# Optimization experiments

Measured on AMD Instinct MI355X. Metric: run time of the kernel, lower is better.

Reference implementation:

```python
import jax, jax.numpy as jnp
import numpy as np

D_MODEL = 1024
HEADS = 4
DK = 1024          # key_dim = d_model * expand_k
DV = 2048          # value_dim = d_model * expand_v
HDK = DK // HEADS  # 256
HDV = DV // HEADS  # 512
LOW_RANK = 16
CHUNK = 64
GATE_NORM = 16.0
EPS = 1e-5


def setup_inputs() -> dict:
    key = jax.random.key(0)
    ks = jax.random.split(key, 10)
    gain = 2.0 ** (-2.5)

    def xavier(k, shape):  # shape = (fan_in, fan_out); stored as [in, out]
        lim = gain * np.sqrt(6.0 / (shape[0] + shape[1]))
        return jax.random.uniform(k, shape, jnp.float32, -lim, lim)

    return {
        'x': jax.random.normal(ks[0], (2, 2048, D_MODEL), jnp.float32),
        'Wq': xavier(ks[1], (D_MODEL, DK)),
        'Wk': xavier(ks[2], (D_MODEL, DK)),
        'Wv': xavier(ks[3], (D_MODEL, DV)),
        'Wg': xavier(ks[4], (D_MODEL, DV)),
        'Wgk1': xavier(ks[5], (D_MODEL, LOW_RANK)),
        'Wgk2': xavier(ks[6], (LOW_RANK, DK)),
        'bgk2': jnp.zeros((DK,), jnp.float32),
        'Wo': xavier(ks[7], (DV, D_MODEL)),
        'rms_w': jnp.ones((HDV,), jnp.float32),
    }


def _gla_chunked(q, k, v, g):
    """Gated linear attention: S_t = exp(g_t) (*) S_{t-1} + k_t^T v_t;  o_t = scale * q_t @ S_t.
    q,k,g: [B,H,T,HDK]; v: [B,H,T,HDV]. Chunk-parallel formulation, scan over chunks."""
    B, H, T, _ = q.shape
    NC = T // CHUNK
    scale = HDK ** -0.5

    def to_chunks(t, d):  # [B,H,T,d] -> [NC,B,H,CHUNK,d]
        return t.reshape(B, H, NC, CHUNK, d).transpose(2, 0, 1, 3, 4)

    qc = to_chunks(q, HDK)
    kc = to_chunks(k, HDK)
    vc = to_chunks(v, HDV)
    bc = jnp.cumsum(to_chunks(g, HDK), axis=-2)  # inclusive log-decay within chunk
    mask = jnp.tril(jnp.ones((CHUNK, CHUNK), bool))

    def step(S, inp):
        qb, kb, vb, bb = inp                       # [B,H,C,HDK/HDV]
        qg = qb * jnp.exp(bb) * scale              # queries decayed to chunk start
        kd = kb * jnp.exp(-bb)                     # keys un-decayed (intra)
        A = jnp.einsum('bhtd,bhsd->bhts', qg, kd)  # intra-chunk scores
        A = jnp.where(mask, A, 0.0)
        o = jnp.einsum('bhts,bhsv->bhtv', A, vb) + jnp.einsum('bhtd,bhdv->bhtv', qg, S)
        b_last = bb[:, :, -1:, :]                  # [B,H,1,HDK]
        kg = kb * jnp.exp(b_last - bb)             # keys decayed to chunk end
        S = S * jnp.exp(b_last[:, :, 0, :])[..., None] + jnp.einsum('bhtd,bhtv->bhdv', kg, vb)
        return S, o

    S0 = jnp.zeros((B, H, HDK, HDV), q.dtype)
    _, o = jax.lax.scan(step, S0, (qc, kc, vc, bc))  # o: [NC,B,H,C,HDV]
    return o.transpose(1, 2, 0, 3, 4).reshape(B, H, T, HDV)


def reference(x, Wq, Wk, Wv, Wg, Wgk1, Wgk2, bgk2, Wo, rms_w):
    B, T, _ = x.shape
    q = (x @ Wq).reshape(B, T, HEADS, HDK).transpose(0, 2, 1, 3)
    k = (x @ Wk).reshape(B, T, HEADS, HDK).transpose(0, 2, 1, 3)
    v = (x @ Wv).reshape(B, T, HEADS, HDV).transpose(0, 2, 1, 3)
    gk = (x @ Wgk1) @ Wgk2 + bgk2                       # low-rank gate logits
    g = jax.nn.log_sigmoid(gk.astype(jnp.float32)) / GATE_NORM
    g = g.reshape(B, T, HEADS, HDK).transpose(0, 2, 1, 3)

    o = _gla_chunked(q, k, v, g)                        # [B,H,T,HDV]
    o = o.transpose(0, 2, 1, 3)                         # [B,T,H,HDV]
    o = o * jax.lax.rsqrt(jnp.mean(o * o, axis=-1, keepdims=True) + EPS) * rms_w
    o = o.reshape(B, T, HEADS * HDV)
    o = o * jax.nn.silu(x @ Wg)
    return o @ Wo
```

## Files before the change

### kernel.cpp

```cpp
#include <hip/hip_runtime.h>
#include <hip/hip_bf16.h>
#include <math.h>

#define TOK  4096
#define DM   1024
#define DKC  1024
#define DVC  2048
#define NH   4
#define HDK_ 256
#define HDV_ 512
#define NCH  32
#define CHK  64

typedef __attribute__((ext_vector_type(8))) short bf16x8;
typedef __attribute__((ext_vector_type(4))) float f32x4;

__device__ inline float bf2f(short s) {
    unsigned int b = ((unsigned int)(unsigned short)s) << 16;
    return __uint_as_float(b);
}
__device__ inline short f2bf_bits(float f) {
    __hip_bfloat16 h = __float2bfloat16(f);
    return *reinterpret_cast<short*>(&h);
}

__device__ __forceinline__ void gl_lds16(const void* g, void* l) {
    __builtin_amdgcn_global_load_lds((const __attribute__((address_space(1))) void*)g,
                                     (__attribute__((address_space(3))) void*)l, 16, 0, 0);
}

__global__ __launch_bounds__(256) void prep_all(const float* __restrict__ Wq,
                                                const float* __restrict__ Wk,
                                                const float* __restrict__ Wv,
                                                const float* __restrict__ Wg,
                                                const float* __restrict__ Wo,
                                                __hip_bfloat16* __restrict__ WtAll,
                                                __hip_bfloat16* __restrict__ WtO,
                                                const float* __restrict__ x,
                                                const float* __restrict__ W1,
                                                const float* __restrict__ W2,
                                                const float* __restrict__ b2,
                                                __hip_bfloat16* __restrict__ xb,
                                                float* __restrict__ g) {
    const int bid = blockIdx.x;
    const int tid = threadIdx.x;
    if (bid < 8192) {
        __shared__ float tile[32][33];
        const float* W; __hip_bfloat16* Wt; int K, N, r;
        if (bid < 1024)      { W = Wq; Wt = WtAll;               K = 1024; N = 1024; r = bid; }
        else if (bid < 2048) { W = Wk; Wt = WtAll + 1024 * 1024; K = 1024; N = 1024; r = bid - 1024; }
        else if (bid < 4096) { W = Wv; Wt = WtAll + 2048 * 1024; K = 1024; N = 2048; r = bid - 2048; }
        else if (bid < 6144) { W = Wg; Wt = WtAll + 4096 * 1024; K = 1024; N = 2048; r = bid - 4096; }
        else                 { W = Wo; Wt = WtO;                 K = 2048; N = 1024; r = bid - 6144; }
        const int ncols = N >> 5;
        const int n0 = (r % ncols) * 32, k0 = (r / ncols) * 32;
        const int tx = tid & 31, ty = tid >> 5;
#pragma unroll
        for (int i = 0; i < 32; i += 8)
            tile[ty + i][tx] = W[(size_t)(k0 + ty + i) * N + n0 + tx];
        __syncthreads();
#pragma unroll
        for (int i = 0; i < 32; i += 8)
            Wt[(size_t)(n0 + ty + i) * K + k0 + tx] = __float2bfloat16(tile[tx][ty + i]);
    } else {
        __shared__ float xl[1024];
        __shared__ float red[16][17];
        __shared__ float t1l[16];
        const int t = bid - 8192;
        float4 xv = *reinterpret_cast<const float4*>(&x[(size_t)t * DM + tid * 4]);
        *reinterpret_cast<float4*>(&xl[tid * 4]) = xv;
        short4 xs;
        xs.x = f2bf_bits(xv.x); xs.y = f2bf_bits(xv.y);
        xs.z = f2bf_bits(xv.z); xs.w = f2bf_bits(xv.w);
        *reinterpret_cast<short4*>((short*)xb + (size_t)t * DM + tid * 4) = xs;
        __syncthreads();
        const int o = tid & 15, p = tid >> 4;
        float s = 0.f;
#pragma unroll 8
        for (int m = 0; m < 64; ++m) {
            int kk = p * 64 + m;
            s += xl[kk] * W1[kk * 16 + o];
        }
        red[p][o] = s;
        __syncthreads();
        if (tid < 16) {
            float tot = 0.f;
#pragma unroll
            for (int pp = 0; pp < 16; ++pp) tot += red[pp][tid];
            t1l[tid] = tot;
        }
        __syncthreads();
#pragma unroll
        for (int j = 0; j < 4; ++j) {
            int c = tid + j * 256;
            float acc = b2[c];
#pragma unroll
            for (int r2 = 0; r2 < 16; ++r2) acc += t1l[r2] * W2[r2 * 1024 + c];
            float ls = fminf(acc, 0.f) - log1pf(expf(-fabsf(acc)));
            g[(size_t)t * DKC + c] = ls * (1.f / 16.f);
        }
    }
}

__global__ __launch_bounds__(512) void gemm256(const __hip_bfloat16* __restrict__ A,
                                               const __hip_bfloat16* __restrict__ Wt,
                                               __hip_bfloat16* __restrict__ qo,
                                               __hip_bfloat16* __restrict__ ko,
                                               __hip_bfloat16* __restrict__ vT,
                                               __hip_bfloat16* __restrict__ xgo) {
    __shared__ __align__(16) short SM[9 * 8192];
    const int K = 1024, NT = 16;
    const int tid = threadIdx.x;
    const int wave = tid >> 6, lane = tid & 63;
    const int wr = wave >> 2;
    const int wc = wave & 3;
    const int hc = wc >> 1;
    const int l15 = lane & 15, kb = lane >> 4;
    const int m0 = blockIdx.y * 128, n0 = blockIdx.x * 256;

    const bool isV = (n0 >= 2048 && n0 < 4096);
    __hip_bfloat16* dst = nullptr; int ldd = 0, nloc0 = 0;
    if (n0 < 1024)       { dst = qo;  ldd = 1024; nloc0 = n0; }
    else if (n0 < 2048)  { dst = ko;  ldd = 1024; nloc0 = n0 - 1024; }
    else if (n0 >= 4096) { dst = xgo; ldd = 2048; nloc0 = n0 - 4096; }

    f32x4 acc[4][4];
#pragma unroll
    for (int mf = 0; mf < 4; ++mf)
#pragma unroll
        for (int nf = 0; nf < 4; ++nf) acc[mf][nf] = (f32x4){0.f, 0.f, 0.f, 0.f};

    auto stage_unit = [&](int u) {
        int tk = u / 3, p = u % 3;
        int slot = u % 9;
#pragma unroll
        for (int j = 0; j < 2; ++j) {
            int row = (wave * 2 + j) * 8 + (lane >> 3);
            int srcg = (lane & 7) ^ (row & 7);
            const __hip_bfloat16* src =
                (p == 0) ? &A[(size_t)(m0 + row) * K + tk * 64 + srcg * 8]
                         : &Wt[(size_t)(n0 + (p - 1) * 128 + row) * K + tk * 64 + srcg * 8];
            gl_lds16(src, &SM[slot * 8192 + (wave * 2 + j) * 512]);
        }
    };

    for (int u = 0; u <= 5; ++u) stage_unit(u);

    const int ULAST = 3 * NT - 1;
    for (int t = 0; t < NT; ++t) {
        if (t < NT - 1) asm volatile("s_waitcnt vmcnt(6)" ::: "memory");
        else            asm volatile("s_waitcnt vmcnt(0)" ::: "memory");
        __builtin_amdgcn_sched_barrier(0);
        __builtin_amdgcn_s_barrier();

        if (3 * t + 6 <= ULAST) stage_unit(3 * t + 6);
        if (3 * t + 7 <= ULAST) stage_unit(3 * t + 7);
        if (3 * t + 8 <= ULAST) stage_unit(3 * t + 8);
        __builtin_amdgcn_sched_barrier(0);

        const short* Abase = &SM[((3 * t) % 9) * 8192];
        const short* Bbase = &SM[((3 * t + 1 + hc) % 9) * 8192];

        bf16x8 a0[4], b0[4], a1[4], b1[4];
#pragma unroll
        for (int mf = 0; mf < 4; ++mf) {
            int row = wr * 64 + mf * 16 + l15;
            a0[mf] = *reinterpret_cast<const bf16x8*>(&Abase[row * 64 + (kb ^ (row & 7)) * 8]);
        }
#pragma unroll
        for (int nf = 0; nf < 4; ++nf) {
            int row = (wc & 1) * 64 + nf * 16 + l15;
            b0[nf] = *reinterpret_cast<const bf16x8*>(&Bbase[row * 64 + (kb ^ (row & 7)) * 8]);
        }
        __builtin_amdgcn_sched_barrier(0);
#pragma unroll
        for (int mf = 0; mf < 4; ++mf) {
            int row = wr * 64 + mf * 16 + l15;
            a1[mf] = *reinterpret_cast<const bf16x8*>(&Abase[row * 64 + ((4 + kb) ^ (row & 7)) * 8]);
        }
#pragma unroll
        for (int nf = 0; nf < 4; ++nf) {
            int row = (wc & 1) * 64 + nf * 16 + l15;
            b1[nf] = *reinterpret_cast<const bf16x8*>(&Bbase[row * 64 + ((4 + kb) ^ (row & 7)) * 8]);
        }
        __builtin_amdgcn_sched_barrier(0);
        asm volatile("s_waitcnt lgkmcnt(8)" ::: "memory");
        __builtin_amdgcn_sched_barrier(0);
        __builtin_amdgcn_s_setprio(1);
#pragma unroll
        for (int mf = 0; mf < 4; ++mf)
#pragma unroll
            for (int nf = 0; nf < 4; ++nf)
                acc[mf][nf] = __builtin_amdgcn_mfma_f32_16x16x32_bf16(a0[mf], b0[nf], acc[mf][nf], 0, 0, 0);
        __builtin_amdgcn_s_setprio(0);
        asm volatile("s_waitcnt lgkmcnt(0)" ::: "memory");
        __builtin_amdgcn_sched_barrier(0);
        __builtin_amdgcn_s_setprio(1);
#pragma unroll
        for (int mf = 0; mf < 4; ++mf)
#pragma unroll
            for (int nf = 0; nf < 4; ++nf)
                acc[mf][nf] = __builtin_amdgcn_mfma_f32_16x16x32_bf16(a1[mf], b1[nf], acc[mf][nf], 0, 0, 0);
        __builtin_amdgcn_s_setprio(0);
    }

    if (!isV) {
#pragma unroll
        for (int mf = 0; mf < 4; ++mf)
#pragma unroll
            for (int nf = 0; nf < 4; ++nf)
#pragma unroll
                for (int r = 0; r < 4; ++r)
                    dst[(size_t)(m0 + wr * 64 + mf * 16 + kb * 4 + r) * ldd +
                        nloc0 + wc * 64 + nf * 16 + l15] = __float2bfloat16(acc[mf][nf][r]);
    } else {
        __syncthreads();
        short* Cl = SM;
#pragma unroll
        for (int mf = 0; mf < 4; ++mf)
#pragma unroll
            for (int nf = 0; nf < 4; ++nf)
#pragma unroll
                for (int r = 0; r < 4; ++r) {
                    int trow = wr * 64 + mf * 16 + kb * 4 + r;
                    int vcol = wc * 64 + nf * 16 + l15;
                    Cl[vcol * 132 + trow] = f2bf_bits(acc[mf][nf][r]);
                }
        __syncthreads();
        const int vcg0 = n0 - 2048;
        const int bh = (m0 >> 11) * NH + (vcg0 >> 9);
        const int vl0 = vcg0 & 511;
        const int tl0 = m0 & 2047;
        short* vTs = (short*)vT;
#pragma unroll
        for (int it = 0; it < 8; ++it) {
            int idx = tid + it * 512;
            int row = idx >> 4;
            int c8 = (idx & 15) * 8;
            bf16x8 vv = *reinterpret_cast<const bf16x8*>(&Cl[row * 132 + c8]);
            *reinterpret_cast<bf16x8*>(
                &vTs[((size_t)(bh * 512 + vl0 + row)) * 2048 + tl0 + c8]) = vv;
        }
    }
}

__global__ __launch_bounds__(256) void gemm_bf16(const __hip_bfloat16* __restrict__ A,
                                                 const __hip_bfloat16* __restrict__ Wt,
                                                 float* __restrict__ C,
                                                 int M, int N, int K) {
    __shared__ __align__(16) short Buf[2][2][128 * 64];
    const int tid = threadIdx.x;
    const int wave = tid >> 6, lane = tid & 63;
    const int wr = wave >> 1, wc = wave & 1;
    const int m0 = blockIdx.y * 128, n0 = blockIdx.x * 128;
    const int l15 = lane & 15, kb = lane >> 4;
    const int lr8 = lane >> 3, lc8 = (lane & 7) * 8;
    const int NT = K >> 6;

    f32x4 acc[4][4];
#pragma unroll
    for (int mf = 0; mf < 4; ++mf)
#pragma unroll
        for (int nf = 0; nf < 4; ++nf) acc[mf][nf] = (f32x4){0.f, 0.f, 0.f, 0.f};

#define STAGE_G(kt, bi)                                                          \
    {                                                                            \
        int k0s = (kt) * 64;                                                     \
        _Pragma("unroll")                                                        \
        for (int j = 0; j < 4; ++j) {                                            \
            int inst = wave * 4 + j;                                             \
            int r = inst * 8 + lr8;                                              \
            gl_lds16(&A[(size_t)(m0 + r) * K + k0s + lc8], &Buf[bi][0][inst * 512]); \
            gl_lds16(&Wt[(size_t)(n0 + r) * K + k0s + lc8], &Buf[bi][1][inst * 512]); \
        }                                                                        \
    }

    STAGE_G(0, 0);
    STAGE_G(1, 1);

    for (int t = 0; t < NT; ++t) {
        if (t + 1 < NT) asm volatile("s_waitcnt vmcnt(8)" ::: "memory");
        else            asm volatile("s_waitcnt vmcnt(0)" ::: "memory");
        __builtin_amdgcn_sched_barrier(0);
        __builtin_amdgcn_s_barrier();
        const short* Ab = Buf[t & 1][0];
        const short* Bb = Buf[t & 1][1];
        bf16x8 a0[4], b0[4], a1[4], b1[4];
#pragma unroll
        for (int mf = 0; mf < 4; ++mf)
            a0[mf] = *reinterpret_cast<const bf16x8*>(&Ab[(wr * 64 + mf * 16 + l15) * 64 + kb * 8]);
#pragma unroll
        for (int nf = 0; nf < 4; ++nf)
            b0[nf] = *reinterpret_cast<const bf16x8*>(&Bb[(wc * 64 + nf * 16 + l15) * 64 + kb * 8]);
        __builtin_amdgcn_sched_barrier(0);
#pragma unroll
        for (int mf = 0; mf < 4; ++mf)
            a1[mf] = *reinterpret_cast<const bf16x8*>(&Ab[(wr * 64 + mf * 16 + l15) * 64 + 32 + kb * 8]);
#pragma unroll
        for (int nf = 0; nf < 4; ++nf)
            b1[nf] = *reinterpret_cast<const bf16x8*>(&Bb[(wc * 64 + nf * 16 + l15) * 64 + 32 + kb * 8]);
        __builtin_amdgcn_sched_barrier(0);
        asm volatile("s_waitcnt lgkmcnt(8)" ::: "memory");
        __builtin_amdgcn_sched_barrier(0);
#pragma unroll
        for (int mf = 0; mf < 4; ++mf)
#pragma unroll
            for (int nf = 0; nf < 4; ++nf)
                acc[mf][nf] = __builtin_amdgcn_mfma_f32_16x16x32_bf16(a0[mf], b0[nf], acc[mf][nf], 0, 0, 0);
        asm volatile("s_waitcnt lgkmcnt(0)" ::: "memory");
        __builtin_amdgcn_sched_barrier(0);
#pragma unroll
        for (int mf = 0; mf < 4; ++mf)
#pragma unroll
            for (int nf = 0; nf < 4; ++nf)
                acc[mf][nf] = __builtin_amdgcn_mfma_f32_16x16x32_bf16(a1[mf], b1[nf], acc[mf][nf], 0, 0, 0);
        __builtin_amdgcn_sched_barrier(0);
        __builtin_amdgcn_s_barrier();
        if (t + 2 < NT) STAGE_G(t + 2, t & 1);
    }
#undef STAGE_G

#pragma unroll
    for (int mf = 0; mf < 4; ++mf)
#pragma unroll
        for (int nf = 0; nf < 4; ++nf)
#pragma unroll
            for (int r = 0; r < 4; ++r)
                C[(size_t)(m0 + wr * 64 + mf * 16 + kb * 4 + r) * N + n0 + wc * 64 + nf * 16 + l15] =
                    acc[mf][nf][r];
}

__global__ __launch_bounds__(256) void gla_chunk(const __hip_bfloat16* __restrict__ qb,
                                                 const __hip_bfloat16* __restrict__ kb,
                                                 const __hip_bfloat16* __restrict__ vT,
                                                 const float* __restrict__ g,
                                                 __hip_bfloat16* __restrict__ qg,
                                                 __hip_bfloat16* __restrict__ U,
                                                 __hip_bfloat16* __restrict__ o1,
                                                 float* __restrict__ dlast) {
    __shared__ __align__(16) short SM[53248];
    short* qg_l = SM;
    short* kd_l = SM + 16384;
    short* V_l  = SM;
    short* kg_l = SM + 32768;
    short* Am_l = SM + 49152;

    const int chunk = blockIdx.x, bh = blockIdx.y;
    const int b = bh >> 2, h = bh & 3;
    const int t0 = b * 2048 + chunk * 64;
    const int tt0 = chunk * 64;
    const int tid = threadIdx.x;
    const float scale = 0.0625f;

    {
        const int d = tid;
        const float* gcol = g + (size_t)t0 * DKC + h * HDK_ + d;
        const __hip_bfloat16* qcol = qb + (size_t)t0 * DKC + h * HDK_ + d;
        const __hip_bfloat16* kcol = kb + (size_t)t0 * DKC + h * HDK_ + d;
        float run = 0.f;
#pragma unroll
        for (int i = 0; i < 64; ++i) run += gcol[(size_t)i * DKC];
        const float ebl = expf(run);
        dlast[((size_t)bh * NCH + chunk) * HDK_ + d] = ebl;

        bf16x8 kreg[8];
        run = 0.f;
#pragma unroll
        for (int i = 0; i < 64; ++i) {
            run += gcol[(size_t)i * DKC];
            float eb = expf(run);
            float qv = __bfloat162float(qcol[(size_t)i * DKC]) * eb * scale;
            float kdv = __bfloat162float(kcol[(size_t)i * DKC]) * expf(-run);
            qg[(size_t)(t0 + i) * DKC + h * HDK_ + d] = __float2bfloat16(qv);
            int bq = ((i * 512 + d * 2) ^ ((i & 7) << 4)) >> 1;
            qg_l[bq] = f2bf_bits(qv);
            kd_l[bq] = f2bf_bits(kdv);
            kreg[i >> 3][i & 7] = f2bf_bits(kdv * ebl);
        }
#pragma unroll
        for (int j = 0; j < 8; ++j)
            *reinterpret_cast<bf16x8*>(&kg_l[d * 64 + ((j ^ (d & 7)) * 8)]) = kreg[j];
    }
    __syncthreads();

    const int wv = tid >> 6, lane = tid & 63;
    const int l15 = lane & 15, kb_ = lane >> 4;

    {
        f32x4 accA[4];
#pragma unroll
        for (int sf = 0; sf < 4; ++sf) accA[sf] = (f32x4){0.f, 0.f, 0.f, 0.f};
        const int trow = wv * 16 + l15;
#pragma unroll
        for (int ks = 0; ks < 8; ++ks) {
            bf16x8 af = *reinterpret_cast<const bf16x8*>(
                &qg_l[((trow * 512 + (ks * 32 + kb_ * 8) * 2) ^ ((trow & 7) << 4)) >> 1]);
#pragma unroll
            for (int sf = 0; sf < 4; ++sf) {
                int srow = sf * 16 + l15;
                bf16x8 bfr = *reinterpret_cast<const bf16x8*>(
                    &kd_l[((srow * 512 + (ks * 32 + kb_ * 8) * 2) ^ ((srow & 7) << 4)) >> 1]);
                accA[sf] = __builtin_amdgcn_mfma_f32_16x16x32_bf16(af, bfr, accA[sf], 0, 0, 0);
            }
        }
#pragma unroll
        for (int sf = 0; sf < 4; ++sf)
#pragma unroll
            for (int r = 0; r < 4; ++r) {
                int t = wv * 16 + kb_ * 4 + r, s = sf * 16 + l15;
                float val = (t >= s) ? accA[sf][r] : 0.f;
                Am_l[((t * 128 + s * 2) ^ ((t & 7) << 4)) >> 1] = f2bf_bits(val);
            }
    }
    __syncthreads();

    {
        const int lr8 = lane >> 3, slot = lane & 7;
#pragma unroll
        for (int i8 = 0; i8 < 16; ++i8) {
            int vrow0 = wv * 128 + i8 * 8;
            const __hip_bfloat16* src =
                &vT[((size_t)bh * 512 + vrow0 + lr8) * 2048 + tt0 + (slot ^ (lr8 & 7)) * 8];
            gl_lds16(src, &V_l[vrow0 * 64]);
        }
    }
    __syncthreads();

    {
        f32x4 accO[4][8];
#pragma unroll
        for (int tf = 0; tf < 4; ++tf)
#pragma unroll
            for (int vf = 0; vf < 8; ++vf) accO[tf][vf] = (f32x4){0.f, 0.f, 0.f, 0.f};
#pragma unroll
        for (int kk = 0; kk < 2; ++kk) {
            bf16x8 af[4];
#pragma unroll
            for (int tf = 0; tf < 4; ++tf) {
                int row = tf * 16 + l15;
                af[tf] = *reinterpret_cast<const bf16x8*>(
                    &Am_l[((row * 128 + (kk * 32 + kb_ * 8) * 2) ^ ((row & 7) << 4)) >> 1]);
            }
#pragma unroll
            for (int vf = 0; vf < 8; ++vf) {
                int rv = wv * 128 + vf * 16 + l15;
                bf16x8 bfr = *reinterpret_cast<const bf16x8*>(
                    &V_l[((rv * 128 + (kk * 32 + kb_ * 8) * 2) ^ ((rv & 7) << 4)) >> 1]);
#pragma unroll
                for (int tf = 0; tf < 4; ++tf)
                    accO[tf][vf] = __builtin_amdgcn_mfma_f32_16x16x32_bf16(af[tf], bfr, accO[tf][vf], 0, 0, 0);
            }
        }
#pragma unroll
        for (int tf = 0; tf < 4; ++tf)
#pragma unroll
            for (int vf = 0; vf < 8; ++vf)
#pragma unroll
                for (int r = 0; r < 4; ++r) {
                    int t = tf * 16 + kb_ * 4 + r;
                    int vv = wv * 128 + vf * 16 + l15;
                    o1[(size_t)(t0 + t) * DVC + h * HDV_ + vv] = __float2bfloat16(accO[tf][vf][r]);
                }
    }

    {
        const size_t Ub = ((size_t)bh * NCH + chunk) * 131072;
        for (int d0 = 0; d0 < 256; d0 += 64) {
            f32x4 accU[8][4];
#pragma unroll
            for (int vf = 0; vf < 8; ++vf)
#pragma unroll
                for (int nf = 0; nf < 4; ++nf) accU[vf][nf] = (f32x4){0.f, 0.f, 0.f, 0.f};
#pragma unroll
            for (int kk = 0; kk < 2; ++kk) {
                bf16x8 av[8], bv[4];
#pragma unroll
                for (int vf = 0; vf < 8; ++vf) {
                    int rv = wv * 128 + vf * 16 + l15;
                    av[vf] = *reinterpret_cast<const bf16x8*>(
                        &V_l[((rv * 128 + (kk * 32 + kb_ * 8) * 2) ^ ((rv & 7) << 4)) >> 1]);
                }
#pragma unroll
                for (int nf = 0; nf < 4; ++nf) {
                    int row = d0 + nf * 16 + l15;
                    bv[nf] = *reinterpret_cast<const bf16x8*>(
                        &kg_l[row * 64 + (((kk * 4 + kb_) ^ (row & 7)) * 8)]);
                }
#pragma unroll
                for (int vf = 0; vf < 8; ++vf)
#pragma unroll
                    for (int nf = 0; nf < 4; ++nf)
                        accU[vf][nf] = __builtin_amdgcn_mfma_f32_16x16x32_bf16(av[vf], bv[nf], accU[vf][nf], 0, 0, 0);
            }
#pragma unroll
            for (int vf = 0; vf < 8; ++vf)
#pragma unroll
                for (int nf = 0; nf < 4; ++nf)
#pragma unroll
                    for (int r = 0; r < 4; ++r) {
                        int vc = wv * 128 + vf * 16 + kb_ * 4 + r;
                        int d = d0 + nf * 16 + l15;
                        U[Ub + (size_t)vc * 256 + d] = __float2bfloat16(accU[vf][nf][r]);
                    }
        }
    }
}

__global__ __launch_bounds__(256) void scan_pass(__hip_bfloat16* __restrict__ U,
                                                 const float* __restrict__ dlast) {
    int gid = blockIdx.x * 256 + threadIdx.x;
    int bh = gid >> 14;
    int rem = gid & 16383;
    int vc = rem >> 5;
    int dg = rem & 31;
    float S[8];
#pragma unroll
    for (int j = 0; j < 8; ++j) S[j] = 0.f;
    size_t base = (size_t)bh * NCH * 131072 + (size_t)vc * 256 + dg * 8;
    for (int c = 0; c < NCH; ++c) {
        __hip_bfloat16* p = U + base + (size_t)c * 131072;
        bf16x8 u = *reinterpret_cast<bf16x8*>(p);
        const float* dl = &dlast[((size_t)bh * NCH + c) * HDK_ + dg * 8];
        float4 e0 = *reinterpret_cast<const float4*>(dl);
        float4 e1 = *reinterpret_cast<const float4*>(dl + 4);
        float e[8] = {e0.x, e0.y, e0.z, e0.w, e1.x, e1.y, e1.z, e1.w};
        bf16x8 outv;
#pragma unroll
        for (int j = 0; j < 8; ++j) {
            outv[j] = f2bf_bits(S[j]);
            S[j] = S[j] * e[j] + bf2f(u[j]);
        }
        *reinterpret_cast<bf16x8*>(p) = outv;
    }
}

__global__ __launch_bounds__(256) void o_pass(const __hip_bfloat16* __restrict__ qg,
                                              const __hip_bfloat16* __restrict__ U,
                                              const __hip_bfloat16* __restrict__ o1,
                                              __hip_bfloat16* __restrict__ o2) {
    __shared__ __align__(16) char smem[64 * 132 * 4];
    short* Av = (short*)smem;
    short* Bv = (short*)smem + 128 * 64;
    float* oT = (float*)smem;
    const int vt = blockIdx.x, c = blockIdx.y, bh = blockIdx.z;
    const int b = bh >> 2, h = bh & 3;
    const int vc0 = vt * 128;
    const int t0 = b * 2048 + c * 64;
    const int tid = threadIdx.x;
    const int wave = tid >> 6, lane = tid & 63;
    const int wr = wave >> 1, wc = wave & 1;
    const int l15 = lane & 15, kb = lane >> 4;
    const int lr8 = lane >> 3, lc8 = (lane & 7) * 8;
    const size_t Ub = ((size_t)bh * NCH + c) * 131072;

    f32x4 acc[4][2];
#pragma unroll
    for (int mf = 0; mf < 4; ++mf)
#pragma unroll
        for (int nf = 0; nf < 2; ++nf) acc[mf][nf] = (f32x4){0.f, 0.f, 0.f, 0.f};

    for (int ks = 0; ks < 4; ++ks) {
        const int d0 = ks * 64;
#pragma unroll
        for (int j = 0; j < 4; ++j) {
            int inst = wave * 4 + j;
            int r = inst * 8 + lr8;
            gl_lds16(&U[Ub + (size_t)(vc0 + r) * 256 + d0 + lc8], &Av[inst * 512]);
        }
#pragma unroll
        for (int j = 0; j < 2; ++j) {
            int inst = wave * 2 + j;
            int r = inst * 8 + lr8;
            gl_lds16(&qg[(size_t)(t0 + r) * DKC + h * HDK_ + d0 + lc8], &Bv[inst * 512]);
        }
        __syncthreads();
#pragma unroll
        for (int kk = 0; kk < 2; ++kk) {
            bf16x8 af[4], bfr[2];
#pragma unroll
            for (int mf = 0; mf < 4; ++mf)
                af[mf] = *reinterpret_cast<const bf16x8*>(&Av[(wr * 64 + mf * 16 + l15) * 64 + kk * 32 + kb * 8]);
#pragma unroll
            for (int nf = 0; nf < 2; ++nf)
                bfr[nf] = *reinterpret_cast<const bf16x8*>(&Bv[(wc * 32 + nf * 16 + l15) * 64 + kk * 32 + kb * 8]);
#pragma unroll
            for (int mf = 0; mf < 4; ++mf)
#pragma unroll
                for (int nf = 0; nf < 2; ++nf)
                    acc[mf][nf] = __builtin_amdgcn_mfma_f32_16x16x32_bf16(af[mf], bfr[nf], acc[mf][nf], 0, 0, 0);
        }
        __syncthreads();
    }
#pragma unroll
    for (int mf = 0; mf < 4; ++mf)
#pragma unroll
        for (int nf = 0; nf < 2; ++nf)
#pragma unroll
            for (int r = 0; r < 4; ++r)
                oT[(wc * 32 + nf * 16 + l15) * 132 + wr * 64 + mf * 16 + kb * 4 + r] = acc[mf][nf][r];
    __syncthreads();
#pragma unroll
    for (int j = 0; j < 4; ++j) {
        int t = (tid >> 4) + j * 16;
        int vc8 = (tid & 15) * 8;
        float4 a0 = *reinterpret_cast<const float4*>(&oT[t * 132 + vc8]);
        float4 a1 = *reinterpret_cast<const float4*>(&oT[t * 132 + vc8 + 4]);
        size_t oi = (size_t)(t0 + t) * DVC + h * HDV_ + vc0 + vc8;
        bf16x8 iv = *reinterpret_cast<const bf16x8*>(&o1[oi]);
        bf16x8 outv;
        outv[0] = f2bf_bits(a0.x + bf2f(iv[0]));
        outv[1] = f2bf_bits(a0.y + bf2f(iv[1]));
        outv[2] = f2bf_bits(a0.z + bf2f(iv[2]));
        outv[3] = f2bf_bits(a0.w + bf2f(iv[3]));
        outv[4] = f2bf_bits(a1.x + bf2f(iv[4]));
        outv[5] = f2bf_bits(a1.y + bf2f(iv[5]));
        outv[6] = f2bf_bits(a1.z + bf2f(iv[6]));
        outv[7] = f2bf_bits(a1.w + bf2f(iv[7]));
        *reinterpret_cast<bf16x8*>((__hip_bfloat16*)o2 + oi) = outv;
    }
}

__global__ __launch_bounds__(256) void rms_gate(const __hip_bfloat16* __restrict__ o2,
                                                const __hip_bfloat16* __restrict__ xg,
                                                const float* __restrict__ rms_w,
                                                __hip_bfloat16* __restrict__ gated) {
    __shared__ float wsum[4];
    const int th = blockIdx.x;
    const int t = th >> 2, h = th & 3;
    const int tid = threadIdx.x;
    const size_t base = (size_t)t * DVC + h * HDV_;
    short2 ov = reinterpret_cast<const short2*>((const short*)o2 + base)[tid];
    float v0 = bf2f(ov.x), v1 = bf2f(ov.y);
    float s = v0 * v0 + v1 * v1;
#pragma unroll
    for (int off = 32; off >= 1; off >>= 1) s += __shfl_down(s, off, 64);
    if ((tid & 63) == 0) wsum[tid >> 6] = s;
    __syncthreads();
    float tot = wsum[0] + wsum[1] + wsum[2] + wsum[3];
    float rms = rsqrtf(tot * (1.f / 512.f) + 1e-5f);
    short2 gv = reinterpret_cast<const short2*>((const short*)xg + base)[tid];
    float g0 = bf2f(gv.x), g1 = bf2f(gv.y);
    float s0 = g0 / (1.f + expf(-g0));
    float s1 = g1 / (1.f + expf(-g1));
    float2 w = reinterpret_cast<const float2*>(rms_w)[tid];
    short2 outp;
    outp.x = f2bf_bits(v0 * rms * w.x * s0);
    outp.y = f2bf_bits(v1 * rms * w.y * s1);
    reinterpret_cast<short2*>((short*)gated + base)[tid] = outp;
}

extern "C" void kernel_launch(void* const* d_in, const int* in_sizes, int n_in,
                              void* d_out, int out_size, void* d_ws, size_t ws_size,
                              hipStream_t stream) {
    const float* x    = (const float*)d_in[0];
    const float* Wq   = (const float*)d_in[1];
    const float* Wk   = (const float*)d_in[2];
    const float* Wv   = (const float*)d_in[3];
    const float* Wg   = (const float*)d_in[4];
    const float* Wgk1 = (const float*)d_in[5];
    const float* Wgk2 = (const float*)d_in[6];
    const float* bgk2 = (const float*)d_in[7];
    const float* Wo   = (const float*)d_in[8];
    const float* rmsw = (const float*)d_in[9];
    float* out = (float*)d_out;
    float* ws = (float*)d_ws;

    const size_t M1 = 1ull << 20;
    __hip_bfloat16* xb    = (__hip_bfloat16*)ws;
    __hip_bfloat16* WtAll = (__hip_bfloat16*)(ws + 2 * M1);
    __hip_bfloat16* q_b   = (__hip_bfloat16*)(ws + 5 * M1);
    __hip_bfloat16* k_b   = (__hip_bfloat16*)(ws + 7 * M1);
    float*          g     = ws + 13 * M1;
    __hip_bfloat16* U     = (__hip_bfloat16*)ws;
    __hip_bfloat16* xg_b  = (__hip_bfloat16*)(ws + 17 * M1);
    __hip_bfloat16* qgb   = (__hip_bfloat16*)(ws + 21 * M1);
    __hip_bfloat16* vT    = (__hip_bfloat16*)(ws + 25 * M1);
    __hip_bfloat16* o1    = (__hip_bfloat16*)(ws + 29 * M1);
    __hip_bfloat16* o2    = (__hip_bfloat16*)(ws + 33 * M1);
    float*          dlast = ws + 37 * M1 + 65536;
    __hip_bfloat16* WtO   = (__hip_bfloat16*)(ws + 38 * M1);
    __hip_bfloat16* gated = (__hip_bfloat16*)(ws + 25 * M1);

    prep_all<<<12288, 256, 0, stream>>>(Wq, Wk, Wv, Wg, Wo, WtAll, WtO,
                                        x, Wgk1, Wgk2, bgk2, xb, g);

    gemm256<<<dim3(24, 32), 512, 0, stream>>>(xb, WtAll, q_b, k_b, vT, xg_b);

    gla_chunk<<<dim3(NCH, 8), 256, 0, stream>>>(q_b, k_b, vT, g, qgb, U, o1, dlast);

    scan_pass<<<512, 256, 0, stream>>>(U, dlast);
    o_pass<<<dim3(4, NCH, 8), 256, 0, stream>>>(qgb, U, o1, o2);

    rms_gate<<<TOK * NH, 256, 0, stream>>>(o2, xg_b, rmsw, gated);
    gemm_bf16<<<dim3(8, 32), 256, 0, stream>>>(gated, WtO, out, TOK, DM, DVC);
}
```

Before: 224.5 us.

## Fuse inter-chunk output pass with RMS norm and SiLU gating

```diff
diff --git a/kernel.cpp b/kernel.cpp
--- a/kernel.cpp
+++ b/kernel.cpp
@@ -534,17 +534,18 @@
     }
 }
 
-__global__ __launch_bounds__(256) void o_pass(const __hip_bfloat16* __restrict__ qg,
+__global__ __launch_bounds__(256) void o_gate(const __hip_bfloat16* __restrict__ qg,
                                               const __hip_bfloat16* __restrict__ U,
                                               const __hip_bfloat16* __restrict__ o1,
-                                              __hip_bfloat16* __restrict__ o2) {
-    __shared__ __align__(16) char smem[64 * 132 * 4];
-    short* Av = (short*)smem;
-    short* Bv = (short*)smem + 128 * 64;
-    float* oT = (float*)smem;
-    const int vt = blockIdx.x, c = blockIdx.y, bh = blockIdx.z;
+                                              const __hip_bfloat16* __restrict__ xg,
+                                              const float* __restrict__ rms_w,
+                                              __hip_bfloat16* __restrict__ gated) {
+    __shared__ __align__(16) short Av[128 * 64];
+    __shared__ __align__(16) short Bv[64 * 64];
+    __shared__ __align__(16) short oT[64 * 520];
+    __shared__ float red[64][4];
+    const int c = blockIdx.x, bh = blockIdx.y;
     const int b = bh >> 2, h = bh & 3;
-    const int vc0 = vt * 128;
     const int t0 = b * 2048 + c * 64;
     const int tid = threadIdx.x;
     const int wave = tid >> 6, lane = tid & 63;
@@ -553,100 +554,102 @@
     const int lr8 = lane >> 3, lc8 = (lane & 7) * 8;
     const size_t Ub = ((size_t)bh * NCH + c) * 131072;
 
-    f32x4 acc[4][2];
-#pragma unroll
-    for (int mf = 0; mf < 4; ++mf)
-#pragma unroll
-        for (int nf = 0; nf < 2; ++nf) acc[mf][nf] = (f32x4){0.f, 0.f, 0.f, 0.f};
-
-    for (int ks = 0; ks < 4; ++ks) {
-        const int d0 = ks * 64;
-#pragma unroll
-        for (int j = 0; j < 4; ++j) {
-            int inst = wave * 4 + j;
-            int r = inst * 8 + lr8;
-            gl_lds16(&U[Ub + (size_t)(vc0 + r) * 256 + d0 + lc8], &Av[inst * 512]);
-        }
-#pragma unroll
-        for (int j = 0; j < 2; ++j) {
-            int inst = wave * 2 + j;
-            int r = inst * 8 + lr8;
-            gl_lds16(&qg[(size_t)(t0 + r) * DKC + h * HDK_ + d0 + lc8], &Bv[inst * 512]);
-        }
-        __syncthreads();
-#pragma unroll
-        for (int kk = 0; kk < 2; ++kk) {
-            bf16x8 af[4], bfr[2];
-#pragma unroll
-            for (int mf = 0; mf < 4; ++mf)
-                af[mf] = *reinterpret_cast<const bf16x8*>(&Av[(wr * 64 + mf * 16 + l15) * 64 + kk * 32 + kb * 8]);
+    for (int vt = 0; vt < 4; ++vt) {
+        const int vc0 = vt * 128;
+        f32x4 acc[4][2];
+#pragma unroll
+        for (int mf = 0; mf < 4; ++mf)
+#pragma unroll
+            for (int nf = 0; nf < 2; ++nf) acc[mf][nf] = (f32x4){0.f, 0.f, 0.f, 0.f};
+
+        for (int ks = 0; ks < 4; ++ks) {
+            const int d0 = ks * 64;
+#pragma unroll
+            for (int j = 0; j < 4; ++j) {
+                int inst = wave * 4 + j;
+                int r = inst * 8 + lr8;
+                gl_lds16(&U[Ub + (size_t)(vc0 + r) * 256 + d0 + lc8], &Av[inst * 512]);
+            }
+#pragma unroll
+            for (int j = 0; j < 2; ++j) {
+                int inst = wave * 2 + j;
+                int r = inst * 8 + lr8;
+                gl_lds16(&qg[(size_t)(t0 + r) * DKC + h * HDK_ + d0 + lc8], &Bv[inst * 512]);
+            }
+            __syncthreads();
+#pragma unroll
+            for (int kk = 0; kk < 2; ++kk) {
+                bf16x8 af[4], bfr[2];
+#pragma unroll
+                for (int mf = 0; mf < 4; ++mf)
+                    af[mf] = *reinterpret_cast<const bf16x8*>(&Av[(wr * 64 + mf * 16 + l15) * 64 + kk * 32 + kb * 8]);
+#pragma unroll
+                for (int nf = 0; nf < 2; ++nf)
+                    bfr[nf] = *reinterpret_cast<const bf16x8*>(&Bv[(wc * 32 + nf * 16 + l15) * 64 + kk * 32 + kb * 8]);
+#pragma unroll
+                for (int mf = 0; mf < 4; ++mf)
+#pragma unroll
+                    for (int nf = 0; nf < 2; ++nf)
+                        acc[mf][nf] = __builtin_amdgcn_mfma_f32_16x16x32_bf16(af[mf], bfr[nf], acc[mf][nf], 0, 0, 0);
+            }
+            __syncthreads();
+        }
+#pragma unroll
+        for (int mf = 0; mf < 4; ++mf)
 #pragma unroll
             for (int nf = 0; nf < 2; ++nf)
-                bfr[nf] = *reinterpret_cast<const bf16x8*>(&Bv[(wc * 32 + nf * 16 + l15) * 64 + kk * 32 + kb * 8]);
-#pragma unroll
-            for (int mf = 0; mf < 4; ++mf)
-#pragma unroll
-                for (int nf = 0; nf < 2; ++nf)
-                    acc[mf][nf] = __builtin_amdgcn_mfma_f32_16x16x32_bf16(af[mf], bfr[nf], acc[mf][nf], 0, 0, 0);
-        }
-        __syncthreads();
-    }
-#pragma unroll
-    for (int mf = 0; mf < 4; ++mf)
-#pragma unroll
-        for (int nf = 0; nf < 2; ++nf)
-#pragma unroll
-            for (int r = 0; r < 4; ++r)
-                oT[(wc * 32 + nf * 16 + l15) * 132 + wr * 64 + mf * 16 + kb * 4 + r] = acc[mf][nf][r];
+#pragma unroll
+                for (int r = 0; r < 4; ++r)
+                    oT[(wc * 32 + nf * 16 + l15) * 520 + vc0 + wr * 64 + mf * 16 + kb * 4 + r] =
+                        f2bf_bits(acc[mf][nf][r]);
+    }
     __syncthreads();
-#pragma unroll
-    for (int j = 0; j < 4; ++j) {
-        int t = (tid >> 4) + j * 16;
-        int vc8 = (tid & 15) * 8;
-        float4 a0 = *reinterpret_cast<const float4*>(&oT[t * 132 + vc8]);
-        float4 a1 = *reinterpret_cast<const float4*>(&oT[t * 132 + vc8 + 4]);
-        size_t oi = (size_t)(t0 + t) * DVC + h * HDV_ + vc0 + vc8;
-        bf16x8 iv = *reinterpret_cast<const bf16x8*>(&o1[oi]);
+
+    {
+        const int row = tid >> 2, q = tid & 3;
+        float s = 0.f;
+        const size_t gbase = (size_t)(t0 + row) * DVC + h * HDV_ + q * 128;
+#pragma unroll
+        for (int j = 0; j < 16; ++j) {
+            bf16x8 ov = *reinterpret_cast<const bf16x8*>(&oT[row * 520 + q * 128 + j * 8]);
+            bf16x8 o1v = *reinterpret_cast<const bf16x8*>(&o1[gbase + j * 8]);
+            bf16x8 o2v;
+#pragma unroll
+            for (int e = 0; e < 8; ++e) {
+                float v = bf2f(ov[e]) + bf2f(o1v[e]);
+                short sb = f2bf_bits(v);
+                o2v[e] = sb;
+                float vb = bf2f(sb);
+                s += vb * vb;
+            }
+            *reinterpret_cast<bf16x8*>(&oT[row * 520 + q * 128 + j * 8]) = o2v;
+        }
+        red[row][q] = s;
+    }
+    __syncthreads();
+
+#pragma unroll
+    for (int it = 0; it < 16; ++it) {
+        int idx = tid + it * 256;
+        int row = idx >> 6;
+        int col8 = (idx & 63) * 8;
+        float tot = red[row][0] + red[row][1] + red[row][2] + red[row][3];
+        float rms = rsqrtf(tot * (1.f / 512.f) + 1e-5f);
+        bf16x8 o2v = *reinterpret_cast<const bf16x8*>(&oT[row * 520 + col8]);
+        const size_t gbase = (size_t)(t0 + row) * DVC + h * HDV_ + col8;
+        bf16x8 xgv = *reinterpret_cast<const bf16x8*>(&xg[gbase]);
+        float4 w0 = *reinterpret_cast<const float4*>(&rms_w[col8]);
+        float4 w1 = *reinterpret_cast<const float4*>(&rms_w[col8 + 4]);
+        float wv[8] = {w0.x, w0.y, w0.z, w0.w, w1.x, w1.y, w1.z, w1.w};
         bf16x8 outv;
-        outv[0] = f2bf_bits(a0.x + bf2f(iv[0]));
-        outv[1] = f2bf_bits(a0.y + bf2f(iv[1]));
-        outv[2] = f2bf_bits(a0.z + bf2f(iv[2]));
-        outv[3] = f2bf_bits(a0.w + bf2f(iv[3]));
-        outv[4] = f2bf_bits(a1.x + bf2f(iv[4]));
-        outv[5] = f2bf_bits(a1.y + bf2f(iv[5]));
-        outv[6] = f2bf_bits(a1.z + bf2f(iv[6]));
-        outv[7] = f2bf_bits(a1.w + bf2f(iv[7]));
-        *reinterpret_cast<bf16x8*>((__hip_bfloat16*)o2 + oi) = outv;
-    }
-}
-
-__global__ __launch_bounds__(256) void rms_gate(const __hip_bfloat16* __restrict__ o2,
-                                                const __hip_bfloat16* __restrict__ xg,
-                                                const float* __restrict__ rms_w,
-                                                __hip_bfloat16* __restrict__ gated) {
-    __shared__ float wsum[4];
-    const int th = blockIdx.x;
-    const int t = th >> 2, h = th & 3;
-    const int tid = threadIdx.x;
-    const size_t base = (size_t)t * DVC + h * HDV_;
-    short2 ov = reinterpret_cast<const short2*>((const short*)o2 + base)[tid];
-    float v0 = bf2f(ov.x), v1 = bf2f(ov.y);
-    float s = v0 * v0 + v1 * v1;
-#pragma unroll
-    for (int off = 32; off >= 1; off >>= 1) s += __shfl_down(s, off, 64);
-    if ((tid & 63) == 0) wsum[tid >> 6] = s;
-    __syncthreads();
-    float tot = wsum[0] + wsum[1] + wsum[2] + wsum[3];
-    float rms = rsqrtf(tot * (1.f / 512.f) + 1e-5f);
-    short2 gv = reinterpret_cast<const short2*>((const short*)xg + base)[tid];
-    float g0 = bf2f(gv.x), g1 = bf2f(gv.y);
-    float s0 = g0 / (1.f + expf(-g0));
-    float s1 = g1 / (1.f + expf(-g1));
-    float2 w = reinterpret_cast<const float2*>(rms_w)[tid];
-    short2 outp;
-    outp.x = f2bf_bits(v0 * rms * w.x * s0);
-    outp.y = f2bf_bits(v1 * rms * w.y * s1);
-    reinterpret_cast<short2*>((short*)gated + base)[tid] = outp;
+#pragma unroll
+        for (int e = 0; e < 8; ++e) {
+            float gv = bf2f(xgv[e]);
+            float sg = gv / (1.f + expf(-gv));
+            outv[e] = f2bf_bits(bf2f(o2v[e]) * rms * wv[e] * sg);
+        }
+        *reinterpret_cast<bf16x8*>((short*)gated + gbase) = outv;
+    }
 }
 
 extern "C" void kernel_launch(void* const* d_in, const int* in_sizes, int n_in,
@@ -676,7 +679,6 @@
     __hip_bfloat16* qgb   = (__hip_bfloat16*)(ws + 21 * M1);
     __hip_bfloat16* vT    = (__hip_bfloat16*)(ws + 25 * M1);
     __hip_bfloat16* o1    = (__hip_bfloat16*)(ws + 29 * M1);
-    __hip_bfloat16* o2    = (__hip_bfloat16*)(ws + 33 * M1);
     float*          dlast = ws + 37 * M1 + 65536;
     __hip_bfloat16* WtO   = (__hip_bfloat16*)(ws + 38 * M1);
     __hip_bfloat16* gated = (__hip_bfloat16*)(ws + 25 * M1);
@@ -689,8 +691,7 @@
     gla_chunk<<<dim3(NCH, 8), 256, 0, stream>>>(q_b, k_b, vT, g, qgb, U, o1, dlast);
 
     scan_pass<<<512, 256, 0, stream>>>(U, dlast);
-    o_pass<<<dim3(4, NCH, 8), 256, 0, stream>>>(qgb, U, o1, o2);
-
-    rms_gate<<<TOK * NH, 256, 0, stream>>>(o2, xg_b, rmsw, gated);
+    o_gate<<<dim3(NCH, 8), 256, 0, stream>>>(qgb, U, o1, xg_b, rmsw, gated);
+
     gemm_bf16<<<dim3(8, 32), 256, 0, stream>>>(gated, WtO, out, TOK, DM, DVC);
 }
```

Result: no change. 225.8 us (+0.6%).
